# Performance work log

Hardware: AMD Instinct MI355X
Metric: run time of the kernel (lower is better)

## Reference

```python
import jax, jax.numpy as jnp
import numpy as np

B, T, I, H = 4096, 128, 32, 64


def _u(key, shape, bound):
    return jax.random.uniform(key, shape, jnp.float32, -bound, bound)


def setup_inputs() -> dict:
    key = jax.random.key(0)
    ks = jax.random.split(key, 14)
    bound = 1.0 / np.sqrt(H)  # torch LSTM/Linear default init scale
    inp = {
        "x": jax.random.normal(ks[0], (B, T, I), jnp.float32),
        "Wih0": _u(ks[1], (4 * H, I), bound),
        "Whh0": _u(ks[2], (4 * H, H), bound),
        "bih0": _u(ks[3], (4 * H,), bound),
        "bhh0": _u(ks[4], (4 * H,), bound),
        "Wih1": _u(ks[5], (4 * H, H), bound),
        "Whh1": _u(ks[6], (4 * H, H), bound),
        "bih1": _u(ks[7], (4 * H,), bound),
        "bhh1": _u(ks[8], (4 * H,), bound),
        "Wc1": _u(ks[9], (32, H), 1.0 / np.sqrt(H)),
        "bc1": _u(ks[10], (32,), 1.0 / np.sqrt(H)),
        "Wc2": _u(ks[11], (1, 32), 1.0 / np.sqrt(32)),
        "bc2": _u(ks[12], (1,), 1.0 / np.sqrt(32)),
    }
    return inp


def lstm_layer(x_tbi, Wih, Whh, bih, bhh):
    """x_tbi: [T, B, in]. Returns (all hidden [T,B,H], final hidden [B,H]).
    PyTorch gate order: i, f, g, o."""
    b = x_tbi.shape[1]
    h0 = jnp.zeros((b, Whh.shape[1]), x_tbi.dtype)
    c0 = jnp.zeros_like(h0)
    # precompute input projections for all timesteps in one big GEMM
    xproj = jnp.einsum('tbi,gi->tbg', x_tbi, Wih) + (bih + bhh)

    def step(carry, xp_t):
        h, c = carry
        gates = xp_t + h @ Whh.T  # [B, 4H]
        i, f, g, o = jnp.split(gates, 4, axis=-1)
        c = jax.nn.sigmoid(f) * c + jax.nn.sigmoid(i) * jnp.tanh(g)
        h = jax.nn.sigmoid(o) * jnp.tanh(c)
        return (h, c), h

    (hT, _), hs = jax.lax.scan(step, (h0, c0), xproj)
    return hs, hT


def reference(x, Wih0, Whh0, bih0, bhh0, Wih1, Whh1, bih1, bhh1, Wc1, bc1, Wc2, bc2):
    x_tbi = jnp.transpose(x, (1, 0, 2))  # [T, B, I]
    hs0, _ = lstm_layer(x_tbi, Wih0, Whh0, bih0, bhh0)
    # dropout between layers is identity in eval mode
    _, hT = lstm_layer(hs0, Wih1, Whh1, bih1, bhh1)  # h_n[-1]: [B, H]
    hidden = jax.nn.relu(hT @ Wc1.T + bc1)  # [B, 32]; classifier dropout = identity (eval)
    out = hidden @ Wc2.T + bc2  # [B, 1]
    return out.squeeze(-1)  # [B]
```

## Files before the change

### kernel.cpp

```cpp
#include <hip/hip_runtime.h>


#define TT 128
#define II 32
#define HH 64

typedef _Float16 half8 __attribute__((ext_vector_type(8)));
typedef float floatx4 __attribute__((ext_vector_type(4)));

#define LOG2E 1.4426950408889634f

__device__ __forceinline__ void bar_lds() {
    asm volatile("s_waitcnt lgkmcnt(0)\n\ts_barrier" ::: "memory");
}

__device__ __forceinline__ half8 load_w_frag(const float* __restrict__ W, int n, int K, int k0) {
    const float* p = W + (size_t)n * K + k0;
    float4 a = *(const float4*)p;
    float4 b = *(const float4*)(p + 4);
    half8 h;
    h[0] = (_Float16)a.x; h[1] = (_Float16)a.y; h[2] = (_Float16)a.z; h[3] = (_Float16)a.w;
    h[4] = (_Float16)b.x; h[5] = (_Float16)b.y; h[6] = (_Float16)b.z; h[7] = (_Float16)b.w;
    return h;
}

__device__ __forceinline__ void cell_update(float gi, float gf, float gg, float go,
                                            float& c, float& h) {
    gi = fminf(fmaxf(gi, -12.f), 12.f);
    gf = fminf(fmaxf(gf, -12.f), 12.f);
    gg = fminf(fmaxf(gg, -12.f), 12.f);
    float u  = __builtin_amdgcn_exp2f(gg * (2.f * LOG2E));
    float vi = __builtin_amdgcn_exp2f(-gi * LOG2E);
    float vf = __builtin_amdgcn_exp2f(-gf * LOG2E);
    float u1 = u + 1.f;
    float D1 = 1.f + vf;
    float D2 = fmaf(vi, u1, u1);
    float R  = __builtin_amdgcn_rcpf(D1 * D2);
    float sigf = R * D2;
    float sit  = (u - 1.f) * (R * D1);
    c = fmaf(sigf, c, sit);
    float cc = fminf(fmaxf(c, -12.f), 12.f);
    float w  = __builtin_amdgcn_exp2f(cc * (2.f * LOG2E));
    float vo = __builtin_amdgcn_exp2f(-go * LOG2E);
    float w1 = w + 1.f;
    float den = fmaf(vo, w1, w1);
    h = (w - 1.f) * __builtin_amdgcn_rcpf(den);
}

__global__ __launch_bounds__(512, 2) void lstm_fused(
    const float* __restrict__ x,
    const float* __restrict__ Wih0, const float* __restrict__ Whh0,
    const float* __restrict__ bih0, const float* __restrict__ bhh0,
    const float* __restrict__ Wih1, const float* __restrict__ Whh1,
    const float* __restrict__ bih1, const float* __restrict__ bhh1,
    const float* __restrict__ Wc1, const float* __restrict__ bc1,
    const float* __restrict__ Wc2, const float* __restrict__ bc2,
    float* __restrict__ out)
{
    __shared__ __align__(16) _Float16 xs[2][16][40];
    __shared__ __align__(16) _Float16 h0s[2][16][72];
    __shared__ __align__(16) _Float16 h1s[2][16][72];
    __shared__ __align__(16) float h1f[16][68];
    __shared__ float hid[16][32];

    const int tid  = threadIdx.x;
    const int wid  = tid >> 6;
    const int w4   = wid & 3;
    const bool isL0 = (wid < 4);
    const int lane = tid & 63;
    const int q  = lane >> 4;
    const int lr = lane & 15;
    const int b0 = blockIdx.x * 16;

    half8 bx0[4], bh0[4][2];
    half8 bi1[4][2], bh1[4][2];
    float biasv[4];
    if (isL0) {
        #pragma unroll
        for (int g = 0; g < 4; ++g) {
            int n = (w4 + 4 * g) * 16 + lr;
            bx0[g]    = load_w_frag(Wih0, n, 32, q * 8);
            bh0[g][0] = load_w_frag(Whh0, n, 64, q * 8);
            bh0[g][1] = load_w_frag(Whh0, n, 64, 32 + q * 8);
            biasv[g]  = bih0[n] + bhh0[n];
        }
    } else {
        #pragma unroll
        for (int g = 0; g < 4; ++g) {
            int n = (w4 + 4 * g) * 16 + lr;
            bi1[g][0] = load_w_frag(Wih1, n, 64, q * 8);
            bi1[g][1] = load_w_frag(Wih1, n, 64, 32 + q * 8);
            bh1[g][0] = load_w_frag(Whh1, n, 64, q * 8);
            bh1[g][1] = load_w_frag(Whh1, n, 64, 32 + q * 8);
            biasv[g]  = bih1[n] + bhh1[n];
        }
    }

    for (int i = tid; i < 2 * 16 * 72; i += 512) {
        ((_Float16*)h0s)[i] = (_Float16)0.0f;
        ((_Float16*)h1s)[i] = (_Float16)0.0f;
    }

    float cr[4] = {0.f, 0.f, 0.f, 0.f};

    const int xm = (tid >> 4) & 15;
    const int xf = (tid & 15) * 2;
    const float* xrow = x + ((size_t)(b0 + xm) * TT) * II + xf;
    float2 xbuf = {0.f, 0.f};
    if (isL0) {
        float2 x0 = *(const float2*)(xrow);
        xs[0][xm][xf]     = (_Float16)x0.x;
        xs[0][xm][xf + 1] = (_Float16)x0.y;
        if (TT > 1) xbuf = *(const float2*)(xrow + 1 * II);
    }

    #pragma unroll 2
    for (int k = 0; k <= TT; ++k) {
        bar_lds();

        const int rd = (k + 1) & 1;
        const int wr = k & 1;
        const bool doL0 = isL0 && (k < TT);
        const bool doL1 = (!isL0) && (k >= 1);
        float hnew[4];
        float2 xnew = xbuf;

        if (doL0) {
            half8 xfrag = *(const half8*)&xs[wr][lr][q * 8];
            half8 h0a   = *(const half8*)&h0s[rd][lr][q * 8];
            half8 h0b   = *(const half8*)&h0s[rd][lr][32 + q * 8];
            if (k + 2 < TT) xnew = *(const float2*)(xrow + (size_t)(k + 2) * II);
            floatx4 a0[4];
            #pragma unroll
            for (int g = 0; g < 4; ++g) {
                floatx4 acc = {biasv[g], biasv[g], biasv[g], biasv[g]};
                acc = __builtin_amdgcn_mfma_f32_16x16x32_f16(xfrag, bx0[g],    acc, 0, 0, 0);
                acc = __builtin_amdgcn_mfma_f32_16x16x32_f16(h0a,   bh0[g][0], acc, 0, 0, 0);
                acc = __builtin_amdgcn_mfma_f32_16x16x32_f16(h0b,   bh0[g][1], acc, 0, 0, 0);
                a0[g] = acc;
            }
            #pragma unroll
            for (int r = 0; r < 4; ++r)
                cell_update(a0[0][r], a0[1][r], a0[2][r], a0[3][r], cr[r], hnew[r]);
        }
        if (doL1) {
            half8 g0a = *(const half8*)&h0s[rd][lr][q * 8];
            half8 g0b = *(const half8*)&h0s[rd][lr][32 + q * 8];
            half8 h1a = *(const half8*)&h1s[rd][lr][q * 8];
            half8 h1b = *(const half8*)&h1s[rd][lr][32 + q * 8];
            floatx4 a1[4];
            #pragma unroll
            for (int g = 0; g < 4; ++g) {
                floatx4 acc = {biasv[g], biasv[g], biasv[g], biasv[g]};
                acc = __builtin_amdgcn_mfma_f32_16x16x32_f16(g0a, bi1[g][0], acc, 0, 0, 0);
                acc = __builtin_amdgcn_mfma_f32_16x16x32_f16(g0b, bi1[g][1], acc, 0, 0, 0);
                acc = __builtin_amdgcn_mfma_f32_16x16x32_f16(h1a, bh1[g][0], acc, 0, 0, 0);
                acc = __builtin_amdgcn_mfma_f32_16x16x32_f16(h1b, bh1[g][1], acc, 0, 0, 0);
                a1[g] = acc;
            }
            #pragma unroll
            for (int r = 0; r < 4; ++r)
                cell_update(a1[0][r], a1[1][r], a1[2][r], a1[3][r], cr[r], hnew[r]);
        }

        if (doL0) {
            #pragma unroll
            for (int r = 0; r < 4; ++r)
                h0s[wr][q * 4 + r][w4 * 16 + lr] = (_Float16)hnew[r];
            if (k + 1 < TT) {
                xs[rd][xm][xf]     = (_Float16)xbuf.x;
                xs[rd][xm][xf + 1] = (_Float16)xbuf.y;
            }
            xbuf = xnew;
        }
        if (doL1) {
            if (k == TT) {
                #pragma unroll
                for (int r = 0; r < 4; ++r)
                    h1f[q * 4 + r][w4 * 16 + lr] = hnew[r];
            } else {
                #pragma unroll
                for (int r = 0; r < 4; ++r)
                    h1s[wr][q * 4 + r][w4 * 16 + lr] = (_Float16)hnew[r];
            }
        }
    }
    __syncthreads();

    if (tid < 256) {
        int m = tid >> 4;
        int u = (tid & 15) * 2;
        float a = bc1[u], b = bc1[u + 1];
        const float* w0 = Wc1 + u * 64;
        const float* w1 = Wc1 + (u + 1) * 64;
        #pragma unroll 8
        for (int kk = 0; kk < 64; ++kk) {
            float hv = h1f[m][kk];
            a += hv * w0[kk];
            b += hv * w1[kk];
        }
        hid[m][u]     = fmaxf(a, 0.f);
        hid[m][u + 1] = fmaxf(b, 0.f);
    }
    __syncthreads();
    if (tid < 16) {
        float o = bc2[0];
        #pragma unroll
        for (int u = 0; u < 32; ++u) o += hid[tid][u] * Wc2[u];
        out[b0 + tid] = o;
    }
}

extern "C" void kernel_launch(void* const* d_in, const int* in_sizes, int n_in,
                              void* d_out, int out_size, void* d_ws, size_t ws_size,
                              hipStream_t stream) {
    (void)in_sizes; (void)n_in; (void)d_ws; (void)ws_size; (void)out_size;
    const float* x    = (const float*)d_in[0];
    const float* Wih0 = (const float*)d_in[1];
    const float* Whh0 = (const float*)d_in[2];
    const float* bih0 = (const float*)d_in[3];
    const float* bhh0 = (const float*)d_in[4];
    const float* Wih1 = (const float*)d_in[5];
    const float* Whh1 = (const float*)d_in[6];
    const float* bih1 = (const float*)d_in[7];
    const float* bhh1 = (const float*)d_in[8];
    const float* Wc1  = (const float*)d_in[9];
    const float* bc1  = (const float*)d_in[10];
    const float* Wc2  = (const float*)d_in[11];
    const float* bc2  = (const float*)d_in[12];
    lstm_fused<<<dim3(256), dim3(512), 0, stream>>>(
        x, Wih0, Whh0, bih0, bhh0, Wih1, Whh1, bih1, bhh1, Wc1, bc1, Wc2, bc2,
        (float*)d_out);
}
```

Baseline: 210.5 us.

## Halve batch per block with transposed MFMA and swizzle-split cell updates

Each block now handles 8 sequences instead of 16, which doubles the grid to 512 blocks and raises launch bounds to 4 blocks per CU. The MFMA operands are swapped so weights are the A operand and hidden state the B operand, with per-row bias vectors. Lanes holding unused rows of the 16-wide tile take the other half's gate values through a ds_swizzle, so every lane runs two cell updates instead of four. The x input is loaded directly into registers, removing its shared-memory staging buffer. The cost is that half of each MFMA computes padding rows, plus extra swizzle traffic.

```diff
diff --git a/kernel.cpp b/kernel.cpp
--- a/kernel.cpp
+++ b/kernel.cpp
@@ -2,22 +2,38 @@
 
 
 #define TT 128
-#define II 32
-#define HH 64
 
 typedef _Float16 half8 __attribute__((ext_vector_type(8)));
+typedef _Float16 half2v __attribute__((ext_vector_type(2)));
 typedef float floatx4 __attribute__((ext_vector_type(4)));
 
 #define LOG2E 1.4426950408889634f
 
 __device__ __forceinline__ void bar_lds() {
     asm volatile("s_waitcnt lgkmcnt(0)\n\ts_barrier" ::: "memory");
+}
+
+__device__ __forceinline__ float swz8(float v) {
+    int i = __builtin_bit_cast(int, v);
+    i = __builtin_amdgcn_ds_swizzle(i, 0x201F);
+    return __builtin_bit_cast(float, i);
+}
+
+__device__ __forceinline__ half2v pk16(float a, float b) {
+    return __builtin_bit_cast(half2v, __builtin_amdgcn_cvt_pkrtz(a, b));
 }
 
 __device__ __forceinline__ half8 load_w_frag(const float* __restrict__ W, int n, int K, int k0) {
     const float* p = W + (size_t)n * K + k0;
     float4 a = *(const float4*)p;
     float4 b = *(const float4*)(p + 4);
+    half8 h;
+    h[0] = (_Float16)a.x; h[1] = (_Float16)a.y; h[2] = (_Float16)a.z; h[3] = (_Float16)a.w;
+    h[4] = (_Float16)b.x; h[5] = (_Float16)b.y; h[6] = (_Float16)b.z; h[7] = (_Float16)b.w;
+    return h;
+}
+
+__device__ __forceinline__ half8 cvt_frag(float4 a, float4 b) {
     half8 h;
     h[0] = (_Float16)a.x; h[1] = (_Float16)a.y; h[2] = (_Float16)a.z; h[3] = (_Float16)a.w;
     h[4] = (_Float16)b.x; h[5] = (_Float16)b.y; h[6] = (_Float16)b.z; h[7] = (_Float16)b.w;
@@ -47,7 +63,7 @@
     h = (w - 1.f) * __builtin_amdgcn_rcpf(den);
 }
 
-__global__ __launch_bounds__(512, 2) void lstm_fused(
+__global__ __launch_bounds__(512, 4) void lstm_fused(
     const float* __restrict__ x,
     const float* __restrict__ Wih0, const float* __restrict__ Whh0,
     const float* __restrict__ bih0, const float* __restrict__ bhh0,
@@ -57,11 +73,10 @@
     const float* __restrict__ Wc2, const float* __restrict__ bc2,
     float* __restrict__ out)
 {
-    __shared__ __align__(16) _Float16 xs[2][16][40];
     __shared__ __align__(16) _Float16 h0s[2][16][72];
     __shared__ __align__(16) _Float16 h1s[2][16][72];
-    __shared__ __align__(16) float h1f[16][68];
-    __shared__ float hid[16][32];
+    __shared__ __align__(16) float h1f[8][68];
+    __shared__ float hid[8][32];
 
     const int tid  = threadIdx.x;
     const int wid  = tid >> 6;
@@ -70,29 +85,36 @@
     const int lane = tid & 63;
     const int q  = lane >> 4;
     const int lr = lane & 15;
-    const int b0 = blockIdx.x * 16;
-
-    half8 bx0[4], bh0[4][2];
-    half8 bi1[4][2], bh1[4][2];
-    float biasv[4];
+    const bool lo8 = (lr < 8);
+    const int br = lr & 7;
+    const int b0 = blockIdx.x * 8;
+
+    half8 wb[4][4];
+    floatx4 binit[4];
     if (isL0) {
         #pragma unroll
         for (int g = 0; g < 4; ++g) {
             int n = (w4 + 4 * g) * 16 + lr;
-            bx0[g]    = load_w_frag(Wih0, n, 32, q * 8);
-            bh0[g][0] = load_w_frag(Whh0, n, 64, q * 8);
-            bh0[g][1] = load_w_frag(Whh0, n, 64, 32 + q * 8);
-            biasv[g]  = bih0[n] + bhh0[n];
+            wb[g][0] = load_w_frag(Wih0, n, 32, q * 8);
+            wb[g][1] = load_w_frag(Whh0, n, 64, q * 8);
+            wb[g][2] = load_w_frag(Whh0, n, 64, 32 + q * 8);
+            int nb = (w4 + 4 * g) * 16 + 4 * q;
+            float4 ba = *(const float4*)&bih0[nb];
+            float4 bb = *(const float4*)&bhh0[nb];
+            binit[g] = floatx4{ba.x + bb.x, ba.y + bb.y, ba.z + bb.z, ba.w + bb.w};
         }
     } else {
         #pragma unroll
         for (int g = 0; g < 4; ++g) {
             int n = (w4 + 4 * g) * 16 + lr;
-            bi1[g][0] = load_w_frag(Wih1, n, 64, q * 8);
-            bi1[g][1] = load_w_frag(Wih1, n, 64, 32 + q * 8);
-            bh1[g][0] = load_w_frag(Whh1, n, 64, q * 8);
-            bh1[g][1] = load_w_frag(Whh1, n, 64, 32 + q * 8);
-            biasv[g]  = bih1[n] + bhh1[n];
+            wb[g][0] = load_w_frag(Wih1, n, 64, q * 8);
+            wb[g][1] = load_w_frag(Wih1, n, 64, 32 + q * 8);
+            wb[g][2] = load_w_frag(Whh1, n, 64, q * 8);
+            wb[g][3] = load_w_frag(Whh1, n, 64, 32 + q * 8);
+            int nb = (w4 + 4 * g) * 16 + 4 * q;
+            float4 ba = *(const float4*)&bih1[nb];
+            float4 bb = *(const float4*)&bhh1[nb];
+            binit[g] = floatx4{ba.x + bb.x, ba.y + bb.y, ba.z + bb.z, ba.w + bb.w};
         }
     }
 
@@ -101,17 +123,18 @@
         ((_Float16*)h1s)[i] = (_Float16)0.0f;
     }
 
-    float cr[4] = {0.f, 0.f, 0.f, 0.f};
-
-    const int xm = (tid >> 4) & 15;
-    const int xf = (tid & 15) * 2;
-    const float* xrow = x + ((size_t)(b0 + xm) * TT) * II + xf;
-    float2 xbuf = {0.f, 0.f};
+    float cr[2] = {0.f, 0.f};
+
+    const int u0 = w4 * 16 + 4 * q + (lo8 ? 0 : 2);
+
+    const float* xlane = x + ((size_t)(b0 + br) * TT) * 32 + q * 8;
+    half8 xcur; float4 xra, xrb;
     if (isL0) {
-        float2 x0 = *(const float2*)(xrow);
-        xs[0][xm][xf]     = (_Float16)x0.x;
-        xs[0][xm][xf + 1] = (_Float16)x0.y;
-        if (TT > 1) xbuf = *(const float2*)(xrow + 1 * II);
+        float4 a0 = *(const float4*)(xlane);
+        float4 a1 = *(const float4*)(xlane + 4);
+        xcur = cvt_frag(a0, a1);
+        xra = *(const float4*)(xlane + 32);
+        xrb = *(const float4*)(xlane + 36);
     }
 
     #pragma unroll 2
@@ -122,88 +145,77 @@
         const int wr = k & 1;
         const bool doL0 = isL0 && (k < TT);
         const bool doL1 = (!isL0) && (k >= 1);
-        float hnew[4];
-        float2 xnew = xbuf;
+        floatx4 a[4];
 
         if (doL0) {
-            half8 xfrag = *(const half8*)&xs[wr][lr][q * 8];
-            half8 h0a   = *(const half8*)&h0s[rd][lr][q * 8];
-            half8 h0b   = *(const half8*)&h0s[rd][lr][32 + q * 8];
-            if (k + 2 < TT) xnew = *(const float2*)(xrow + (size_t)(k + 2) * II);
-            floatx4 a0[4];
+            half8 hb0a = *(const half8*)&h0s[rd][lr][q * 8];
+            half8 hb0b = *(const half8*)&h0s[rd][lr][32 + q * 8];
+            half8 xnxt = cvt_frag(xra, xrb);
+            int t2 = (k + 2 < TT) ? (k + 2) : (TT - 1);
+            xra = *(const float4*)(xlane + (size_t)t2 * 32);
+            xrb = *(const float4*)(xlane + (size_t)t2 * 32 + 4);
             #pragma unroll
             for (int g = 0; g < 4; ++g) {
-                floatx4 acc = {biasv[g], biasv[g], biasv[g], biasv[g]};
-                acc = __builtin_amdgcn_mfma_f32_16x16x32_f16(xfrag, bx0[g],    acc, 0, 0, 0);
-                acc = __builtin_amdgcn_mfma_f32_16x16x32_f16(h0a,   bh0[g][0], acc, 0, 0, 0);
-                acc = __builtin_amdgcn_mfma_f32_16x16x32_f16(h0b,   bh0[g][1], acc, 0, 0, 0);
-                a0[g] = acc;
-            }
-            #pragma unroll
-            for (int r = 0; r < 4; ++r)
-                cell_update(a0[0][r], a0[1][r], a0[2][r], a0[3][r], cr[r], hnew[r]);
+                floatx4 acc = binit[g];
+                acc = __builtin_amdgcn_mfma_f32_16x16x32_f16(wb[g][0], xcur, acc, 0, 0, 0);
+                acc = __builtin_amdgcn_mfma_f32_16x16x32_f16(wb[g][1], hb0a, acc, 0, 0, 0);
+                acc = __builtin_amdgcn_mfma_f32_16x16x32_f16(wb[g][2], hb0b, acc, 0, 0, 0);
+                a[g] = acc;
+            }
+            xcur = xnxt;
         }
         if (doL1) {
             half8 g0a = *(const half8*)&h0s[rd][lr][q * 8];
             half8 g0b = *(const half8*)&h0s[rd][lr][32 + q * 8];
             half8 h1a = *(const half8*)&h1s[rd][lr][q * 8];
             half8 h1b = *(const half8*)&h1s[rd][lr][32 + q * 8];
-            floatx4 a1[4];
             #pragma unroll
             for (int g = 0; g < 4; ++g) {
-                floatx4 acc = {biasv[g], biasv[g], biasv[g], biasv[g]};
-                acc = __builtin_amdgcn_mfma_f32_16x16x32_f16(g0a, bi1[g][0], acc, 0, 0, 0);
-                acc = __builtin_amdgcn_mfma_f32_16x16x32_f16(g0b, bi1[g][1], acc, 0, 0, 0);
-                acc = __builtin_amdgcn_mfma_f32_16x16x32_f16(h1a, bh1[g][0], acc, 0, 0, 0);
-                acc = __builtin_amdgcn_mfma_f32_16x16x32_f16(h1b, bh1[g][1], acc, 0, 0, 0);
-                a1[g] = acc;
-            }
+                floatx4 acc = binit[g];
+                acc = __builtin_amdgcn_mfma_f32_16x16x32_f16(wb[g][0], g0a, acc, 0, 0, 0);
+                acc = __builtin_amdgcn_mfma_f32_16x16x32_f16(wb[g][1], g0b, acc, 0, 0, 0);
+                acc = __builtin_amdgcn_mfma_f32_16x16x32_f16(wb[g][2], h1a, acc, 0, 0, 0);
+                acc = __builtin_amdgcn_mfma_f32_16x16x32_f16(wb[g][3], h1b, acc, 0, 0, 0);
+                a[g] = acc;
+            }
+        }
+
+        if (doL0 || doL1) {
+            float v0[4], v1[4];
             #pragma unroll
-            for (int r = 0; r < 4; ++r)
-                cell_update(a1[0][r], a1[1][r], a1[2][r], a1[3][r], cr[r], hnew[r]);
-        }
-
-        if (doL0) {
-            #pragma unroll
-            for (int r = 0; r < 4; ++r)
-                h0s[wr][q * 4 + r][w4 * 16 + lr] = (_Float16)hnew[r];
-            if (k + 1 < TT) {
-                xs[rd][xm][xf]     = (_Float16)xbuf.x;
-                xs[rd][xm][xf + 1] = (_Float16)xbuf.y;
-            }
-            xbuf = xnew;
-        }
-        if (doL1) {
-            if (k == TT) {
-                #pragma unroll
-                for (int r = 0; r < 4; ++r)
-                    h1f[q * 4 + r][w4 * 16 + lr] = hnew[r];
+            for (int g = 0; g < 4; ++g) {
+                float s2 = swz8(a[g][2]);
+                float s3 = swz8(a[g][3]);
+                v0[g] = lo8 ? a[g][0] : s2;
+                v1[g] = lo8 ? a[g][1] : s3;
+            }
+            float hv0, hv1;
+            cell_update(v0[0], v0[1], v0[2], v0[3], cr[0], hv0);
+            cell_update(v1[0], v1[1], v1[2], v1[3], cr[1], hv1);
+
+            if (doL0) {
+                *(half2v*)&h0s[wr][br][u0] = pk16(hv0, hv1);
+            } else if (k == TT) {
+                *(float2*)&h1f[br][u0] = float2{hv0, hv1};
             } else {
-                #pragma unroll
-                for (int r = 0; r < 4; ++r)
-                    h1s[wr][q * 4 + r][w4 * 16 + lr] = (_Float16)hnew[r];
+                *(half2v*)&h1s[wr][br][u0] = pk16(hv0, hv1);
             }
         }
     }
     __syncthreads();
 
     if (tid < 256) {
-        int m = tid >> 4;
-        int u = (tid & 15) * 2;
-        float a = bc1[u], b = bc1[u + 1];
+        int m = tid >> 5;
+        int u = tid & 31;
+        float acc = bc1[u];
         const float* w0 = Wc1 + u * 64;
-        const float* w1 = Wc1 + (u + 1) * 64;
         #pragma unroll 8
-        for (int kk = 0; kk < 64; ++kk) {
-            float hv = h1f[m][kk];
-            a += hv * w0[kk];
-            b += hv * w1[kk];
-        }
-        hid[m][u]     = fmaxf(a, 0.f);
-        hid[m][u + 1] = fmaxf(b, 0.f);
+        for (int kk = 0; kk < 64; ++kk)
+            acc += h1f[m][kk] * w0[kk];
+        hid[m][u] = fmaxf(acc, 0.f);
     }
     __syncthreads();
-    if (tid < 16) {
+    if (tid < 8) {
         float o = bc2[0];
         #pragma unroll
         for (int u = 0; u < 32; ++u) o += hid[tid][u] * Wc2[u];
@@ -228,7 +240,7 @@
     const float* bc1  = (const float*)d_in[10];
     const float* Wc2  = (const float*)d_in[11];
     const float* bc2  = (const float*)d_in[12];
-    lstm_fused<<<dim3(256), dim3(512), 0, stream>>>(
+    lstm_fused<<<dim3(512), dim3(512), 0, stream>>>(
         x, Wih0, Whh0, bih0, bhh0, Wih1, Whh1, bih1, bhh1, Wc1, bc1, Wc2, bc2,
         (float*)d_out);
 }
```

New measurement: 357.2 us. 69.7% more time.
